# Kernel tuning notes

Hardware: AMD Instinct MI355X
Metric: run time of the kernel (lower is better)

Reference implementation:

```python
import jax, jax.numpy as jnp
import numpy as np

D_MODEL = 128
NUM_CLASSES = 32
ETA = 4.0
RC = 6.0
NR = 4          # ceil(D_MODEL / NUM_CLASSES)
# lmax = floor(sqrt(NR-1)) = 1 -> spherical harmonics l=0 and l=1 (4 components)


def setup_inputs() -> dict:
    key = jax.random.key(0)
    k1, k2 = jax.random.split(key)
    B, N = 256, 1024
    xyz = jax.random.normal(k1, (B, N, 3), dtype=jnp.float32) * 2.0
    cls = jax.random.randint(k2, (B, N), 0, NUM_CLASSES).astype(jnp.float32)
    x = jnp.concatenate([xyz, cls[..., None]], axis=-1)  # [B,N,4]
    return {"x": x}


def _forward(x):
    Rs = jnp.arange(NR, dtype=x.dtype) * (RC / NR)       # [NR] = [0,1.5,3,4.5]
    xyz = x[..., :3]
    r = jnp.sqrt(jnp.sum(xyz * xyz, axis=-1))            # [B,N]

    # radial basis: exp(-eta*(Rs - r)^2)                  -> [B,N,NR]
    radial = jnp.exp(-ETA * (Rs - r[..., None]) ** 2)

    # cosine cutoff (r clamped to Rc -> weight 0 beyond)  -> [B,N,1]
    rc = jnp.minimum(r, RC)
    env = (0.5 * jnp.cos(jnp.pi * rc / RC) + 0.5)[..., None]

    # real spherical harmonics l<=1 on unit directions, orthonormal norm,
    # m ordering (-l..l): [Y00, Y1,-1~y, Y1,0~z, Y1,1~x]  -> [B,N,NR]
    u = xyz / jnp.where(r > 0, r, 1.0)[..., None]
    y00 = 0.5 / jnp.sqrt(jnp.pi)
    c1 = jnp.sqrt(3.0 / (4.0 * jnp.pi))
    sh = jnp.stack(
        [jnp.full(r.shape, y00, dtype=x.dtype),
         c1 * u[..., 1], c1 * u[..., 2], c1 * u[..., 0]], axis=-1)

    prod = sh * radial * env                             # [B,N,NR]

    # per-class masked scatter: pos[b,n,:,c] = prod[b,n,:] where class==c and r!=0
    cls = x[..., 3].astype(jnp.int32)
    onehot = jax.nn.one_hot(cls, NUM_CLASSES, dtype=prod.dtype) * (r != 0)[..., None]
    pos = prod[..., :, None] * onehot[..., None, :]      # [B,N,NR,C]
    B, N = x.shape[0], x.shape[1]
    pos = pos.reshape(B, N, NR * NUM_CLASSES)[..., :D_MODEL]

    pos = jnp.nan_to_num(pos, nan=0.0)

    # torch F.normalize default dim=1 (neighbor axis), eps=1e-12
    norm = jnp.sqrt(jnp.sum(pos * pos, axis=1, keepdims=True))
    pos = pos / jnp.maximum(norm, 1e-12)

    # standardize along feature axis (torch std is unbiased, ddof=1)
    mean = jnp.mean(pos, axis=-1, keepdims=True)
    std = jnp.std(pos, axis=-1, ddof=1, keepdims=True)
    return (pos - mean) / (std + 1e-6)


def reference(x):
    return _forward(x)
```

## Files before the change

### kernel.cpp

```cpp
#include <hip/hip_runtime.h>
#include <math.h>

#define B_SZ 256
#define N_SZ 1024
#define D_MODEL 128
#define NUM_CLASSES 32
#define NR 4

#define K_EXP (-5.770780163555854f)
#define K_COS (1.0f / 12.0f)

__device__ __forceinline__ void compute_prod(const float4 xv, float& r, int& c, float p[4]) {
    const float y00 = 0.28209479177387814f;
    const float c1  = 0.48860251190291992f;
    float r2 = xv.x * xv.x + xv.y * xv.y + xv.z * xv.z;
    r = sqrtf(r2);
    c = (int)xv.w;
    float inv_r = (r > 0.0f) ? __builtin_amdgcn_rcpf(r) : 0.0f;
    float ux = xv.x * inv_r, uy = xv.y * inv_r, uz = xv.z * inv_r;
    float rc = fminf(r, 6.0f);
    float env = 0.5f * __builtin_amdgcn_cosf(rc * K_COS) + 0.5f;
    float d0 = 0.0f - r, d1 = 1.5f - r, d2 = 3.0f - r, d3 = 4.5f - r;
    float rad0 = __builtin_amdgcn_exp2f(d0 * d0 * K_EXP);
    float rad1 = __builtin_amdgcn_exp2f(d1 * d1 * K_EXP);
    float rad2 = __builtin_amdgcn_exp2f(d2 * d2 * K_EXP);
    float rad3 = __builtin_amdgcn_exp2f(d3 * d3 * K_EXP);
    p[0] = y00 * rad0 * env;
    p[1] = c1 * uy * rad1 * env;
    p[2] = c1 * uz * rad2 * env;
    p[3] = c1 * ux * rad3 * env;
}

__global__ __launch_bounds__(1024) void ape_norm_kernel(const float* __restrict__ x,
                                                        float* __restrict__ inv_norm) {
    __shared__ float nsq[D_MODEL];
    const int b = blockIdx.x;
    const int t = threadIdx.x;
    if (t < D_MODEL) nsq[t] = 0.0f;
    __syncthreads();
    float4 xv = ((const float4*)x)[(size_t)b * N_SZ + t];
    float r; int c; float p[4];
    compute_prod(xv, r, c, p);
    if (r > 0.0f) {
        atomicAdd(&nsq[0 * NUM_CLASSES + c], p[0] * p[0]);
        atomicAdd(&nsq[1 * NUM_CLASSES + c], p[1] * p[1]);
        atomicAdd(&nsq[2 * NUM_CLASSES + c], p[2] * p[2]);
        atomicAdd(&nsq[3 * NUM_CLASSES + c], p[3] * p[3]);
    }
    __syncthreads();
    if (t < D_MODEL) {
        float nv = sqrtf(nsq[t]);
        inv_norm[b * D_MODEL + t] = __builtin_amdgcn_rcpf(fmaxf(nv, 1e-12f));
    }
}

__global__ __launch_bounds__(256) void ape_main_kernel(const float* __restrict__ x,
                                                       const float* __restrict__ inv_norm,
                                                       float* __restrict__ out) {
    const int gid = blockIdx.x * 256 + threadIdx.x;
    const int pt = gid >> 2;
    const int sub = gid & 3;
    const int b = pt >> 10;

    const float4 xv = ((const float4*)x)[pt];
    float r; int c; float p[4];
    compute_prod(xv, r, c, p);

    float bneg = 0.0f;
    float amb[4] = {0.0f, 0.0f, 0.0f, 0.0f};
    if (r > 0.0f) {
        const float* nb = inv_norm + b * D_MODEL + c;
        float pn0 = p[0] * nb[0];
        float pn1 = p[1] * nb[32];
        float pn2 = p[2] * nb[64];
        float pn3 = p[3] * nb[96];
        float sum = pn0 + pn1 + pn2 + pn3;
        float mean = sum * (1.0f / 128.0f);
        float sumsq = pn0 * pn0 + pn1 * pn1 + pn2 * pn2 + pn3 * pn3;
        float var = (sumsq - 128.0f * mean * mean) * (1.0f / 127.0f);
        var = fmaxf(var, 0.0f);
        float inv_std = __builtin_amdgcn_rcpf(sqrtf(var) + 1e-6f);
        bneg = -mean * inv_std;
        amb[0] = pn0 * inv_std + bneg;
        amb[1] = pn1 * inv_std + bneg;
        amb[2] = pn2 * inv_std + bneg;
        amb[3] = pn3 * inv_std + bneg;
    }
    float4* ob = (float4*)out + (size_t)pt * 32 + sub;
    const int hb = sub * 4;
#pragma unroll
    for (int j = 0; j < 8; ++j) {
        const float a = amb[j >> 1];
        const int cb = (j & 1) * 16 + hb;
        float4 o;
        o.x = (cb + 0 == c) ? a : bneg;
        o.y = (cb + 1 == c) ? a : bneg;
        o.z = (cb + 2 == c) ? a : bneg;
        o.w = (cb + 3 == c) ? a : bneg;
        ob[j * 4] = o;
    }
}

extern "C" void kernel_launch(void* const* d_in, const int* in_sizes, int n_in,
                              void* d_out, int out_size, void* d_ws, size_t ws_size,
                              hipStream_t stream) {
    const float* x = (const float*)d_in[0];
    float* out = (float*)d_out;
    float* inv_norm = (float*)d_ws;

    ape_norm_kernel<<<B_SZ, 1024, 0, stream>>>(x, inv_norm);

    const int total_threads = B_SZ * N_SZ * 4;
    ape_main_kernel<<<total_threads / 256, 256, 0, stream>>>(x, inv_norm, out);
}
```

Baseline: 140.1 us.

## Fuse norm and output kernels into one per-batch block kernel

Merges the column-norm reduction and the output standardization into a single kernel with one 1024-thread block per batch. Per-point products and classes are staged in shared memory, so the input is read and the products computed only once, and the workspace round trip plus the second launch go away. In exchange the grid is only 256 blocks, and each block is large and uses more shared memory. That may limit occupancy and overlap for the write-bound 128 MB output store.

```diff
diff --git a/kernel.cpp b/kernel.cpp
--- a/kernel.cpp
+++ b/kernel.cpp
@@ -5,7 +5,6 @@
 #define N_SZ 1024
 #define D_MODEL 128
 #define NUM_CLASSES 32
-#define NR 4
 
 #define K_EXP (-5.770780163555854f)
 #define K_COS (1.0f / 12.0f)
@@ -31,73 +30,73 @@
     p[3] = c1 * ux * rad3 * env;
 }
 
-__global__ __launch_bounds__(1024) void ape_norm_kernel(const float* __restrict__ x,
-                                                        float* __restrict__ inv_norm) {
+__global__ __launch_bounds__(1024) void ape_fused_kernel(const float* __restrict__ x,
+                                                         float* __restrict__ out) {
     __shared__ float nsq[D_MODEL];
+    __shared__ float invn[D_MODEL];
+    __shared__ float sp0[N_SZ], sp1[N_SZ], sp2[N_SZ], sp3[N_SZ];
+    __shared__ int   scls[N_SZ];
+
     const int b = blockIdx.x;
     const int t = threadIdx.x;
     if (t < D_MODEL) nsq[t] = 0.0f;
     __syncthreads();
-    float4 xv = ((const float4*)x)[(size_t)b * N_SZ + t];
-    float r; int c; float p[4];
-    compute_prod(xv, r, c, p);
-    if (r > 0.0f) {
-        atomicAdd(&nsq[0 * NUM_CLASSES + c], p[0] * p[0]);
-        atomicAdd(&nsq[1 * NUM_CLASSES + c], p[1] * p[1]);
-        atomicAdd(&nsq[2 * NUM_CLASSES + c], p[2] * p[2]);
-        atomicAdd(&nsq[3 * NUM_CLASSES + c], p[3] * p[3]);
+
+    {
+        float4 xv = ((const float4*)x)[(size_t)b * N_SZ + t];
+        float r; int c; float p[4];
+        compute_prod(xv, r, c, p);
+        if (r <= 0.0f) { p[0] = p[1] = p[2] = p[3] = 0.0f; }
+        sp0[t] = p[0]; sp1[t] = p[1]; sp2[t] = p[2]; sp3[t] = p[3];
+        scls[t] = c;
+        if (r > 0.0f) {
+            atomicAdd(&nsq[0 * NUM_CLASSES + c], p[0] * p[0]);
+            atomicAdd(&nsq[1 * NUM_CLASSES + c], p[1] * p[1]);
+            atomicAdd(&nsq[2 * NUM_CLASSES + c], p[2] * p[2]);
+            atomicAdd(&nsq[3 * NUM_CLASSES + c], p[3] * p[3]);
+        }
     }
     __syncthreads();
+
     if (t < D_MODEL) {
-        float nv = sqrtf(nsq[t]);
-        inv_norm[b * D_MODEL + t] = __builtin_amdgcn_rcpf(fmaxf(nv, 1e-12f));
+        invn[t] = __builtin_amdgcn_rcpf(fmaxf(sqrtf(nsq[t]), 1e-12f));
     }
-}
+    __syncthreads();
 
-__global__ __launch_bounds__(256) void ape_main_kernel(const float* __restrict__ x,
-                                                       const float* __restrict__ inv_norm,
-                                                       float* __restrict__ out) {
-    const int gid = blockIdx.x * 256 + threadIdx.x;
-    const int pt = gid >> 2;
-    const int sub = gid & 3;
-    const int b = pt >> 10;
-
-    const float4 xv = ((const float4*)x)[pt];
-    float r; int c; float p[4];
-    compute_prod(xv, r, c, p);
-
-    float bneg = 0.0f;
-    float amb[4] = {0.0f, 0.0f, 0.0f, 0.0f};
-    if (r > 0.0f) {
-        const float* nb = inv_norm + b * D_MODEL + c;
-        float pn0 = p[0] * nb[0];
-        float pn1 = p[1] * nb[32];
-        float pn2 = p[2] * nb[64];
-        float pn3 = p[3] * nb[96];
+    const int sub = t & 3;
+    const int hb = sub * 4;
+#pragma unroll
+    for (int k = 0; k < 4; ++k) {
+        const int n = k * 256 + (t >> 2);
+        const int c = scls[n];
+        float pn0 = sp0[n] * invn[0 * NUM_CLASSES + c];
+        float pn1 = sp1[n] * invn[1 * NUM_CLASSES + c];
+        float pn2 = sp2[n] * invn[2 * NUM_CLASSES + c];
+        float pn3 = sp3[n] * invn[3 * NUM_CLASSES + c];
         float sum = pn0 + pn1 + pn2 + pn3;
         float mean = sum * (1.0f / 128.0f);
         float sumsq = pn0 * pn0 + pn1 * pn1 + pn2 * pn2 + pn3 * pn3;
-        float var = (sumsq - 128.0f * mean * mean) * (1.0f / 127.0f);
-        var = fmaxf(var, 0.0f);
+        float var = fmaxf((sumsq - 128.0f * mean * mean) * (1.0f / 127.0f), 0.0f);
         float inv_std = __builtin_amdgcn_rcpf(sqrtf(var) + 1e-6f);
-        bneg = -mean * inv_std;
+        float bneg = -mean * inv_std;
+        float amb[4];
         amb[0] = pn0 * inv_std + bneg;
         amb[1] = pn1 * inv_std + bneg;
         amb[2] = pn2 * inv_std + bneg;
         amb[3] = pn3 * inv_std + bneg;
-    }
-    float4* ob = (float4*)out + (size_t)pt * 32 + sub;
-    const int hb = sub * 4;
+
+        float4* ob = (float4*)out + ((size_t)b * N_SZ + n) * 32 + sub;
 #pragma unroll
-    for (int j = 0; j < 8; ++j) {
-        const float a = amb[j >> 1];
-        const int cb = (j & 1) * 16 + hb;
-        float4 o;
-        o.x = (cb + 0 == c) ? a : bneg;
-        o.y = (cb + 1 == c) ? a : bneg;
-        o.z = (cb + 2 == c) ? a : bneg;
-        o.w = (cb + 3 == c) ? a : bneg;
-        ob[j * 4] = o;
+        for (int j = 0; j < 8; ++j) {
+            const float a = amb[j >> 1];
+            const int cb = (j & 1) * 16 + hb;
+            float4 o;
+            o.x = (cb + 0 == c) ? a : bneg;
+            o.y = (cb + 1 == c) ? a : bneg;
+            o.z = (cb + 2 == c) ? a : bneg;
+            o.w = (cb + 3 == c) ? a : bneg;
+            ob[j * 4] = o;
+        }
     }
 }
 
@@ -106,10 +105,5 @@
                               hipStream_t stream) {
     const float* x = (const float*)d_in[0];
     float* out = (float*)d_out;
-    float* inv_norm = (float*)d_ws;
-
-    ape_norm_kernel<<<B_SZ, 1024, 0, stream>>>(x, inv_norm);
-
-    const int total_threads = B_SZ * N_SZ * 4;
-    ape_main_kernel<<<total_threads / 256, 256, 0, stream>>>(x, inv_norm, out);
+    ape_fused_kernel<<<B_SZ, 1024, 0, stream>>>(x, out);
 }
```

After: 138.6 us. No clear change (-1.1%).
